# Kernel optimization log

Measured on AMD Instinct MI355X. Metric: run time of the kernel, lower is better.

The kernel has to match this reference:

```python
import jax, jax.numpy as jnp
import numpy as np


def setup_inputs() -> dict:
    key = jax.random.key(0)
    ks = jax.random.split(key, 6)
    B, H, W, C = 4, 56, 56, 256
    NH, K = 8, 7
    return {
        "x": jax.random.normal(ks[0], (B, H, W, C), dtype=jnp.float32),
        "w_qkv": jax.random.normal(ks[1], (C, 3 * C), dtype=jnp.float32) * 0.02,
        "b_qkv": jax.random.normal(ks[2], (3 * C,), dtype=jnp.float32) * 0.02,
        "rpb": jax.random.normal(ks[3], (NH, K * K), dtype=jnp.float32) * 0.02,
        "w_proj": jax.random.normal(ks[4], (C, C), dtype=jnp.float32) * 0.02,
        "b_proj": jax.random.normal(ks[5], (C,), dtype=jnp.float32) * 0.02,
    }


def _window_stack(xp, H, W, ks):
    # xp: (B, H+2p, W+2p, nh, hd) zero-padded map.
    # Returns (B, H, W, nh, ks*ks, hd): each pixel's ks x ks neighborhood,
    # row-major (h offset outer, w offset inner) to match torch unfold order.
    return jnp.stack(
        [xp[:, i:i + H, j:j + W] for i in range(ks) for j in range(ks)],
        axis=-2,
    )


def reference(x, w_qkv, b_qkv, rpb, w_proj, b_proj):
    B, H, W, C = x.shape
    nh, ks2 = rpb.shape
    ks = int(np.sqrt(ks2) + 0.5)  # 7
    hd = C // nh
    scale = hd ** -0.5
    pad = ks // 2  # dilation == 1

    qkv = (x @ w_qkv + b_qkv).reshape(B, H, W, 3, nh, hd)
    q = qkv[..., 0, :, :] * scale        # (B,H,W,nh,hd)
    k = qkv[..., 1, :, :]
    v = qkv[..., 2, :, :]

    pads = ((0, 0), (pad, pad), (pad, pad), (0, 0), (0, 0))
    kw = _window_stack(jnp.pad(k, pads), H, W, ks)  # (B,H,W,nh,ks2,hd)
    vw = _window_stack(jnp.pad(v, pads), H, W, ks)

    # scores over each pixel's ks*ks neighbors (zero-padded borders kept,
    # matching the torch reference), plus relative position bias.
    attn = jnp.einsum("bhwnd,bhwnkd->bhwnk", q, kw) + rpb[None, None, None]
    attn = jax.nn.softmax(attn, axis=-1)
    out = jnp.einsum("bhwnk,bhwnkd->bhwnd", attn, vw).reshape(B, H, W, C)
    return out @ w_proj + b_proj
```

## Files before the change

kernel.cpp:

```cpp
#include <hip/hip_runtime.h>
#include <hip/hip_bf16.h>


using frag_ab = __attribute__((ext_vector_type(8))) short;
using f32x4   = __attribute__((ext_vector_type(4))) float;
using f32x2   = __attribute__((ext_vector_type(2))) float;

typedef const __attribute__((address_space(1))) unsigned int* gas_u32;
typedef __attribute__((address_space(3))) unsigned int*       las_u32;

__device__ __forceinline__ void gl_lds16(const void* g, void* l) {
    __builtin_amdgcn_global_load_lds((gas_u32)g, (las_u32)l, 16, 0, 0);
}

__device__ __forceinline__ float bflo(unsigned int u) { return __uint_as_float(u << 16); }
__device__ __forceinline__ float bfhi(unsigned int u) { return __uint_as_float(u & 0xffff0000u); }

__device__ __forceinline__ f32x2 unpk2(unsigned int u) {
    f32x2 r; r.x = bflo(u); r.y = bfhi(u); return r;
}

#if defined(__has_builtin)
#if __has_builtin(__builtin_amdgcn_fdot2_f32_bf16)
#define HAVE_FDOT2_BF16 1
#endif
#endif

#ifdef HAVE_FDOT2_BF16
typedef __bf16 bf16x2 __attribute__((ext_vector_type(2)));
__device__ __forceinline__ float dot2bf(unsigned int a, unsigned int b, float c) {
    union { unsigned int u; bf16x2 h; } ua, ub;
    ua.u = a; ub.u = b;
    return __builtin_amdgcn_fdot2_f32_bf16(ua.h, ub.h, c, false);
}
#endif

__global__ __launch_bounds__(256) void prep(
    const float* __restrict__ x,      __hip_bfloat16* __restrict__ xb,
    const float* __restrict__ w_qkv,  __hip_bfloat16* __restrict__ wqkvT,
    const float* __restrict__ w_proj, __hip_bfloat16* __restrict__ wprojT,
    __hip_bfloat16* __restrict__ kp,  __hip_bfloat16* __restrict__ vp)
{
    const int bid = blockIdx.x;
    const int tid = threadIdx.x;
    if (bid < 3136) {
        const int i = bid * 256 + tid;
        const float4 v = ((const float4*)x)[i];
        union { ushort4 u; __hip_bfloat16 h[4]; } o;
        o.h[0] = __float2bfloat16(v.x); o.h[1] = __float2bfloat16(v.y);
        o.h[2] = __float2bfloat16(v.z); o.h[3] = __float2bfloat16(v.w);
        ((ushort4*)xb)[i] = o.u;
    } else if (bid < 3904) {
        const int idx = (bid - 3136) * 256 + tid;
        const int k = idx & 255, n = idx >> 8;
        wqkvT[idx] = __float2bfloat16(w_qkv[k * 768 + n]);
    } else if (bid < 4160) {
        const int idx = (bid - 3904) * 256 + tid;
        const int k = idx & 255, n = idx >> 8;
        wprojT[idx] = __float2bfloat16(w_proj[k * 256 + n]);
    } else {
        const int u    = (bid - 4160) * 256 + tid;
        const int ip   = u / 30720;
        const int rem  = u - ip * 30720;
        const int cloc = rem >> 5;
        const int q16  = rem & 31;
        const int img  = ip >> 1;
        __hip_bfloat16* base = (ip & 1) ? vp : kp;
        int prow, pcol;
        if (cloc < 512) {
            const int r8 = cloc >> 6;
            prow = (r8 < 3) ? r8 : r8 + 56;
            pcol = cloc & 63;
        } else {
            const int c2 = cloc - 512;
            prow = 3 + (c2 >> 3);
            const int cc = c2 & 7;
            pcol = (cc < 3) ? cc : cc + 56;
        }
        *(uint4*)(base + (((size_t)(img * 64 + prow)) * 64 + pcol) * 256 + q16 * 8) =
            make_uint4(0u, 0u, 0u, 0u);
    }
}

#define GEMM128_BODY(EPILOGUE)                                                  \
    constexpr int K = 256;                                                      \
    __shared__ frag_ab As[8][64];                                     \
    __shared__ frag_ab Bs[8][64];                                     \
    const int tid  = threadIdx.x;                                               \
    const int lane = tid & 63;                                                  \
    const int w    = tid >> 6;                                                  \
    const int wm   = w >> 1, wn = w & 1;                                        \
    const int m0 = blockIdx.y * 128;                                            \
    const int n0 = blockIdx.x * 128;                                            \
    const int lrow = lane & 15;                                                 \
    const int lk   = (lane >> 4) * 8;                                           \
    const __hip_bfloat16* gA0 = A  + (size_t)(m0 + (2*w+0)*16 + lrow) * K + lk; \
    const __hip_bfloat16* gA1 = A  + (size_t)(m0 + (2*w+1)*16 + lrow) * K + lk; \
    const __hip_bfloat16* gB0 = BT + (size_t)(n0 + (2*w+0)*16 + lrow) * K + lk; \
    const __hip_bfloat16* gB1 = BT + (size_t)(n0 + (2*w+1)*16 + lrow) * K + lk; \
    f32x4 acc[4][4] = {};                                                       \
    for (int k0 = 0; k0 < K; k0 += 32) {                                        \
        gl_lds16(gA0 + k0, &As[2*w+0][0]);                                      \
        gl_lds16(gA1 + k0, &As[2*w+1][0]);                                      \
        gl_lds16(gB0 + k0, &Bs[2*w+0][0]);                                      \
        gl_lds16(gB1 + k0, &Bs[2*w+1][0]);                                      \
        __syncthreads();                                                        \
        frag_ab af[4], bf[4];                                                   \
        _Pragma("unroll")                                                       \
        for (int i = 0; i < 4; ++i) { af[i] = As[wm*4+i][lane]; bf[i] = Bs[wn*4+i][lane]; } \
        _Pragma("unroll")                                                       \
        for (int i = 0; i < 4; ++i)                                             \
            _Pragma("unroll")                                                   \
            for (int j = 0; j < 4; ++j)                                         \
                acc[i][j] = __builtin_amdgcn_mfma_f32_16x16x32_bf16(af[i], bf[j], acc[i][j], 0, 0, 0); \
        __syncthreads();                                                        \
    }                                                                           \
    const int rbase = (lane >> 4) * 4;                                          \
    const int cbase = lane & 15;                                                \
    _Pragma("unroll")                                                           \
    for (int fi = 0; fi < 4; ++fi) {                                            \
        const int rm = m0 + wm * 64 + fi * 16 + rbase;                          \
        _Pragma("unroll")                                                       \
        for (int fj = 0; fj < 4; ++fj) {                                        \
            const int cn = n0 + wn * 64 + fj * 16 + cbase;                      \
            const float bv = bias[cn];                                          \
            _Pragma("unroll")                                                   \
            for (int r = 0; r < 4; ++r) {                                       \
                const int m = rm + r;                                           \
                const float val = acc[fi][fj][r] + bv;                          \
                EPILOGUE                                                        \
            }                                                                   \
        }                                                                       \
    }

__global__ __launch_bounds__(256) void gemm_qkv(
    const __hip_bfloat16* __restrict__ A,
    const __hip_bfloat16* __restrict__ BT,
    const float* __restrict__ bias,
    __hip_bfloat16* __restrict__ qf,
    __hip_bfloat16* __restrict__ kp,
    __hip_bfloat16* __restrict__ vp,
    float qscale)
{
    GEMM128_BODY({
        const int sel = cn >> 8;
        if (sel == 0) {
            qf[(size_t)m * 256 + cn] = __float2bfloat16(val * qscale);
        } else {
            const int c  = cn & 255;
            const int b  = m / 3136;
            const int r2 = m % 3136;
            const int yy = r2 / 56;
            const int xx = r2 % 56;
            __hip_bfloat16* dst = (sel == 1) ? kp : vp;
            dst[(((size_t)(b * 64 + yy + 3)) * 64 + (xx + 3)) * 256 + c] =
                __float2bfloat16(val);
        }
    })
}

__global__ __launch_bounds__(256) void gemm_proj(
    const __hip_bfloat16* __restrict__ A,
    const __hip_bfloat16* __restrict__ BT,
    const float* __restrict__ bias,
    float* __restrict__ C)
{
    constexpr int K = 256;
    __shared__ frag_ab As[4][64];
    __shared__ frag_ab Bs[4][64];

    const int tid  = threadIdx.x;
    const int lane = tid & 63;
    const int w    = tid >> 6;
    const int wm   = w >> 1, wn = w & 1;
    const int m0 = blockIdx.y * 64;
    const int n0 = blockIdx.x * 64;

    const int lrow = lane & 15;
    const int lk   = (lane >> 4) * 8;
    const __hip_bfloat16* gA = A  + (size_t)(m0 + w * 16 + lrow) * K + lk;
    const __hip_bfloat16* gB = BT + (size_t)(n0 + w * 16 + lrow) * K + lk;

    f32x4 acc[2][2] = {};

    for (int k0 = 0; k0 < K; k0 += 32) {
        gl_lds16(gA + k0, &As[w][0]);
        gl_lds16(gB + k0, &Bs[w][0]);
        __syncthreads();
        const frag_ab a0 = As[2 * wm + 0][lane];
        const frag_ab a1 = As[2 * wm + 1][lane];
        const frag_ab b0 = Bs[2 * wn + 0][lane];
        const frag_ab b1 = Bs[2 * wn + 1][lane];
        acc[0][0] = __builtin_amdgcn_mfma_f32_16x16x32_bf16(a0, b0, acc[0][0], 0, 0, 0);
        acc[0][1] = __builtin_amdgcn_mfma_f32_16x16x32_bf16(a0, b1, acc[0][1], 0, 0, 0);
        acc[1][0] = __builtin_amdgcn_mfma_f32_16x16x32_bf16(a1, b0, acc[1][0], 0, 0, 0);
        acc[1][1] = __builtin_amdgcn_mfma_f32_16x16x32_bf16(a1, b1, acc[1][1], 0, 0, 0);
        __syncthreads();
    }

    const int rbase = (lane >> 4) * 4;
    const int cbase = lane & 15;
    #pragma unroll
    for (int fi = 0; fi < 2; ++fi) {
        const int rm = m0 + wm * 32 + fi * 16 + rbase;
        #pragma unroll
        for (int fj = 0; fj < 2; ++fj) {
            const int cn = n0 + wn * 32 + fj * 16 + cbase;
            const float bv = bias[cn];
            #pragma unroll
            for (int r = 0; r < 4; ++r)
                C[(size_t)(rm + r) * 256 + cn] = acc[fi][fj][r] + bv;
        }
    }
}

__global__ __launch_bounds__(64) void na2d_attn11(
    const __hip_bfloat16* __restrict__ qf,
    const __hip_bfloat16* __restrict__ kp,
    const __hip_bfloat16* __restrict__ vp,
    const float* __restrict__ rpb,
    __hip_bfloat16* __restrict__ out)
{
    const int lane = threadIdx.x;
    const int half = lane & 1;
    const int h    = (lane >> 1) & 7;
    const int tl   = (lane >> 4) & 3;

    const int bid = blockIdx.x;
    const int seg = (bid & 7) * 392 + (bid >> 3);
    const int row = seg / 14;
    const int x0  = (seg % 14) * 4;
    const int b   = row / 56;
    const int y   = row % 56;
    const int t   = row * 56 + x0 + tl;
    const int prow0 = b * 64 + y;

    __shared__ __hip_bfloat16 kbuf[10 * 264];
    __shared__ float srpb[8 * 49];

    for (int i = lane; i < 8 * 49; i += 64) srpb[i] = rpb[i];
    __syncthreads();

    unsigned int qpk[8];
    {
        const uint4* qp = (const uint4*)(qf + (size_t)t * 256 + h * 32 + half * 16);
        const uint4 qa = qp[0], qb = qp[1];
        qpk[0] = qa.x; qpk[1] = qa.y; qpk[2] = qa.z; qpk[3] = qa.w;
        qpk[4] = qb.x; qpk[5] = qb.y; qpk[6] = qb.z; qpk[7] = qb.w;
    }
#ifndef HAVE_FDOT2_BF16
    f32x2 q2[8];
    #pragma unroll
    for (int i = 0; i < 8; ++i) q2[i] = unpk2(qpk[i]);
#endif

    const int wroff = (lane >> 5) * 528 + (lane & 31) * 16;
    const int rdoff = tl * 528 + h * 64 + half * 32;

#define GLOAD(plane, ky, d0, d1, d2, d3, d4)                                    \
    do {                                                                        \
        const char* rb_ = (const char*)((plane) +                               \
            ((size_t)(prow0 + (ky)) * 64 + x0) * 256 + lane * 8);               \
        d0 = *(const uint4*)(rb_);                                              \
        d1 = *(const uint4*)(rb_ + 1024);                                       \
        d2 = *(const uint4*)(rb_ + 2048);                                       \
        d3 = *(const uint4*)(rb_ + 3072);                                       \
        d4 = *(const uint4*)(rb_ + 4096);                                       \
    } while (0)

#define LWRITE(buf, s0, s1, s2, s3, s4)                                         \
    do {                                                                        \
        char* wb_ = (char*)(buf) + wroff;                                       \
        *(uint4*)(wb_)        = s0;                                             \
        *(uint4*)(wb_ + 1056) = s1;                                             \
        *(uint4*)(wb_ + 2112) = s2;                                             \
        *(uint4*)(wb_ + 3168) = s3;                                             \
        *(uint4*)(wb_ + 4224) = s4;                                             \
    } while (0)

    const float* rp = &srpb[h * 49];
    float m = -1e30f, l = 0.f;
    f32x2 o2[8] = {};

    uint4 k0, k1, k2, k3, k4;
    GLOAD(kp, 0, k0, k1, k2, k3, k4);

    #pragma unroll 1
    for (int ky = 0; ky < 7; ++ky) {
        LWRITE(kbuf, k0, k1, k2, k3, k4);
        const __hip_bfloat16* vrow = vp +
            ((size_t)(prow0 + ky) * 64 + x0 + tl) * 256 + h * 32 + half * 16;
        uint4 va[7], vb[7];
        #pragma unroll
        for (int kx = 0; kx < 7; ++kx) {
            va[kx] = *(const uint4*)(vrow + kx * 256);
            vb[kx] = *(const uint4*)(vrow + kx * 256 + 8);
        }
        if (ky < 6) GLOAD(kp, ky + 1, k0, k1, k2, k3, k4);
        float lg[7];
        #pragma unroll
        for (int kx = 0; kx < 7; ++kx) {
            const uint4* p = (const uint4*)((const char*)kbuf + rdoff + kx * 528);
            const uint4 w0 = p[0];
            const uint4 w1 = p[1];
#ifdef HAVE_FDOT2_BF16
            float s = 0.f;
            s = dot2bf(qpk[0], w0.x, s);
            s = dot2bf(qpk[1], w0.y, s);
            s = dot2bf(qpk[2], w0.z, s);
            s = dot2bf(qpk[3], w0.w, s);
            s = dot2bf(qpk[4], w1.x, s);
            s = dot2bf(qpk[5], w1.y, s);
            s = dot2bf(qpk[6], w1.z, s);
            s = dot2bf(qpk[7], w1.w, s);
#else
            f32x2 s2 = {0.f, 0.f};
            s2 += q2[0] * unpk2(w0.x);
            s2 += q2[1] * unpk2(w0.y);
            s2 += q2[2] * unpk2(w0.z);
            s2 += q2[3] * unpk2(w0.w);
            s2 += q2[4] * unpk2(w1.x);
            s2 += q2[5] * unpk2(w1.y);
            s2 += q2[6] * unpk2(w1.z);
            s2 += q2[7] * unpk2(w1.w);
            const float s = s2.x + s2.y;
#endif
            lg[kx] = s;
        }
        #pragma unroll
        for (int kx = 0; kx < 7; ++kx) {
            lg[kx] += __shfl_xor(lg[kx], 1, 64);
            lg[kx] += rp[ky * 7 + kx];
        }
        float rmax = lg[0];
        #pragma unroll
        for (int kx = 1; kx < 7; ++kx) rmax = fmaxf(rmax, lg[kx]);
        const float mnew  = fmaxf(m, rmax);
        const float alpha = __expf(m - mnew);
        m = mnew;
        l *= alpha;
        const f32x2 alpha2 = {alpha, alpha};
        #pragma unroll
        for (int i = 0; i < 8; ++i) o2[i] *= alpha2;
        #pragma unroll
        for (int kx = 0; kx < 7; ++kx) {
            const float pr = __expf(lg[kx] - mnew);
            l += pr;
            const f32x2 pr2 = {pr, pr};
            const uint4 w0 = va[kx];
            const uint4 w1 = vb[kx];
            o2[0] += pr2 * unpk2(w0.x);
            o2[1] += pr2 * unpk2(w0.y);
            o2[2] += pr2 * unpk2(w0.z);
            o2[3] += pr2 * unpk2(w0.w);
            o2[4] += pr2 * unpk2(w1.x);
            o2[5] += pr2 * unpk2(w1.y);
            o2[6] += pr2 * unpk2(w1.z);
            o2[7] += pr2 * unpk2(w1.w);
        }
    }
#undef GLOAD
#undef LWRITE

    const float inv = 1.f / l;
    union { uint4 u[2]; __hip_bfloat16 hh[16]; } ob;
    #pragma unroll
    for (int i = 0; i < 8; ++i) {
        ob.hh[2 * i + 0] = __float2bfloat16(o2[i].x * inv);
        ob.hh[2 * i + 1] = __float2bfloat16(o2[i].y * inv);
    }
    uint4* op = (uint4*)(out + (size_t)t * 256 + h * 32 + half * 16);
    op[0] = ob.u[0];
    op[1] = ob.u[1];
}

extern "C" void kernel_launch(void* const* d_in, const int* in_sizes, int n_in,
                              void* d_out, int out_size, void* d_ws, size_t ws_size,
                              hipStream_t stream)
{
    const float* x      = (const float*)d_in[0];
    const float* w_qkv  = (const float*)d_in[1];
    const float* b_qkv  = (const float*)d_in[2];
    const float* rpb    = (const float*)d_in[3];
    const float* w_proj = (const float*)d_in[4];
    const float* b_proj = (const float*)d_in[5];
    float* out = (float*)d_out;

    const int M = 12544;

    char* wsp = (char*)d_ws;
    __hip_bfloat16* qf    = (__hip_bfloat16*)wsp; wsp += (size_t)M * 256 * 2;
    __hip_bfloat16* kp    = (__hip_bfloat16*)wsp; wsp += (size_t)4 * 64 * 64 * 256 * 2;
    __hip_bfloat16* vp    = (__hip_bfloat16*)wsp; wsp += (size_t)4 * 64 * 64 * 256 * 2;
    __hip_bfloat16* xb    = (__hip_bfloat16*)wsp; wsp += (size_t)M * 256 * 2;
    __hip_bfloat16* attnb = (__hip_bfloat16*)wsp; wsp += (size_t)M * 256 * 2;
    __hip_bfloat16* wqkvT = (__hip_bfloat16*)wsp; wsp += (size_t)768 * 256 * 2;
    __hip_bfloat16* wprojT= (__hip_bfloat16*)wsp; wsp += (size_t)256 * 256 * 2;

    const float scale = 0.17677669529663689f;

    prep<<<5120, 256, 0, stream>>>(x, xb, w_qkv, wqkvT, w_proj, wprojT, kp, vp);

    gemm_qkv<<<dim3(6, 98), 256, 0, stream>>>(xb, wqkvT, b_qkv, qf, kp, vp, scale);

    na2d_attn11<<<3136, 64, 0, stream>>>(qf, kp, vp, rpb, attnb);

    gemm_proj<<<dim3(4, 196), 256, 0, stream>>>(attnb, wprojT, b_proj, out);
}
```

Measured before the change: 133.0 us.

## Split head dim across four lanes, two pixels per block in neighborhood attention

Each attention wave now covers 2 pixels instead of 4. Each head's 32-dim slice is split across 4 lanes of 8 elements rather than 2 lanes of 16, and the grid is doubled to 6272 blocks. This halves per-thread registers for V prefetch and accumulators, which may raise occupancy and latency hiding. The cost is an extra cross-lane shuffle per logit and less K-row reuse per block, since each block now loads an 8-pixel row segment to serve 2 outputs instead of 10 for 4.

```diff
diff --git a/kernel.cpp b/kernel.cpp
--- a/kernel.cpp
+++ b/kernel.cpp
@@ -214,7 +214,7 @@
     }
 }
 
-__global__ __launch_bounds__(64) void na2d_attn11(
+__global__ __launch_bounds__(64) void na2d_attn12(
     const __hip_bfloat16* __restrict__ qf,
     const __hip_bfloat16* __restrict__ kp,
     const __hip_bfloat16* __restrict__ vp,
@@ -222,42 +222,40 @@
     __hip_bfloat16* __restrict__ out)
 {
     const int lane = threadIdx.x;
-    const int half = lane & 1;
-    const int h    = (lane >> 1) & 7;
-    const int tl   = (lane >> 4) & 3;
+    const int q8   = lane & 3;
+    const int h    = (lane >> 2) & 7;
+    const int tl   = (lane >> 5) & 1;
 
     const int bid = blockIdx.x;
-    const int seg = (bid & 7) * 392 + (bid >> 3);
-    const int row = seg / 14;
-    const int x0  = (seg % 14) * 4;
+    const int seg = (bid & 7) * 784 + (bid >> 3);
+    const int row = seg / 28;
+    const int x0  = (seg % 28) * 2;
     const int b   = row / 56;
     const int y   = row % 56;
     const int t   = row * 56 + x0 + tl;
     const int prow0 = b * 64 + y;
 
-    __shared__ __hip_bfloat16 kbuf[10 * 264];
+    __shared__ __hip_bfloat16 kbuf[8 * 256];
     __shared__ float srpb[8 * 49];
 
     for (int i = lane; i < 8 * 49; i += 64) srpb[i] = rpb[i];
     __syncthreads();
 
-    unsigned int qpk[8];
+    unsigned int qpk[4];
     {
-        const uint4* qp = (const uint4*)(qf + (size_t)t * 256 + h * 32 + half * 16);
-        const uint4 qa = qp[0], qb = qp[1];
+        const uint4 qa = *(const uint4*)(qf + (size_t)t * 256 + h * 32 + q8 * 8);
         qpk[0] = qa.x; qpk[1] = qa.y; qpk[2] = qa.z; qpk[3] = qa.w;
-        qpk[4] = qb.x; qpk[5] = qb.y; qpk[6] = qb.z; qpk[7] = qb.w;
     }
 #ifndef HAVE_FDOT2_BF16
-    f32x2 q2[8];
+    f32x2 q2[4];
     #pragma unroll
-    for (int i = 0; i < 8; ++i) q2[i] = unpk2(qpk[i]);
-#endif
-
-    const int wroff = (lane >> 5) * 528 + (lane & 31) * 16;
-    const int rdoff = tl * 528 + h * 64 + half * 32;
-
-#define GLOAD(plane, ky, d0, d1, d2, d3, d4)                                    \
+    for (int i = 0; i < 4; ++i) q2[i] = unpk2(qpk[i]);
+#endif
+
+    const int wroff = lane * 16;
+    const int rdoff = tl * 512 + h * 64 + q8 * 16;
+
+#define GLOAD(plane, ky, d0, d1, d2, d3)                                        \
     do {                                                                        \
         const char* rb_ = (const char*)((plane) +                               \
             ((size_t)(prow0 + (ky)) * 64 + x0) * 256 + lane * 8);               \
@@ -265,64 +263,50 @@
         d1 = *(const uint4*)(rb_ + 1024);                                       \
         d2 = *(const uint4*)(rb_ + 2048);                                       \
         d3 = *(const uint4*)(rb_ + 3072);                                       \
-        d4 = *(const uint4*)(rb_ + 4096);                                       \
     } while (0)
 
-#define LWRITE(buf, s0, s1, s2, s3, s4)                                         \
+#define LWRITE(buf, s0, s1, s2, s3)                                             \
     do {                                                                        \
         char* wb_ = (char*)(buf) + wroff;                                       \
         *(uint4*)(wb_)        = s0;                                             \
-        *(uint4*)(wb_ + 1056) = s1;                                             \
-        *(uint4*)(wb_ + 2112) = s2;                                             \
-        *(uint4*)(wb_ + 3168) = s3;                                             \
-        *(uint4*)(wb_ + 4224) = s4;                                             \
+        *(uint4*)(wb_ + 1024) = s1;                                             \
+        *(uint4*)(wb_ + 2048) = s2;                                             \
+        *(uint4*)(wb_ + 3072) = s3;                                             \
     } while (0)
 
     const float* rp = &srpb[h * 49];
     float m = -1e30f, l = 0.f;
-    f32x2 o2[8] = {};
-
-    uint4 k0, k1, k2, k3, k4;
-    GLOAD(kp, 0, k0, k1, k2, k3, k4);
+    f32x2 o2[4] = {};
+
+    uint4 k0, k1, k2, k3;
+    GLOAD(kp, 0, k0, k1, k2, k3);
 
     #pragma unroll 1
     for (int ky = 0; ky < 7; ++ky) {
-        LWRITE(kbuf, k0, k1, k2, k3, k4);
+        LWRITE(kbuf, k0, k1, k2, k3);
         const __hip_bfloat16* vrow = vp +
-            ((size_t)(prow0 + ky) * 64 + x0 + tl) * 256 + h * 32 + half * 16;
-        uint4 va[7], vb[7];
+            ((size_t)(prow0 + ky) * 64 + x0 + tl) * 256 + h * 32 + q8 * 8;
+        uint4 va[7];
+        #pragma unroll
+        for (int kx = 0; kx < 7; ++kx)
+            va[kx] = *(const uint4*)(vrow + kx * 256);
+        if (ky < 6) GLOAD(kp, ky + 1, k0, k1, k2, k3);
+        float lg[7];
         #pragma unroll
         for (int kx = 0; kx < 7; ++kx) {
-            va[kx] = *(const uint4*)(vrow + kx * 256);
-            vb[kx] = *(const uint4*)(vrow + kx * 256 + 8);
-        }
-        if (ky < 6) GLOAD(kp, ky + 1, k0, k1, k2, k3, k4);
-        float lg[7];
-        #pragma unroll
-        for (int kx = 0; kx < 7; ++kx) {
-            const uint4* p = (const uint4*)((const char*)kbuf + rdoff + kx * 528);
-            const uint4 w0 = p[0];
-            const uint4 w1 = p[1];
+            const uint4 w0 = *(const uint4*)((const char*)kbuf + rdoff + kx * 512);
 #ifdef HAVE_FDOT2_BF16
             float s = 0.f;
             s = dot2bf(qpk[0], w0.x, s);
             s = dot2bf(qpk[1], w0.y, s);
             s = dot2bf(qpk[2], w0.z, s);
             s = dot2bf(qpk[3], w0.w, s);
-            s = dot2bf(qpk[4], w1.x, s);
-            s = dot2bf(qpk[5], w1.y, s);
-            s = dot2bf(qpk[6], w1.z, s);
-            s = dot2bf(qpk[7], w1.w, s);
 #else
             f32x2 s2 = {0.f, 0.f};
             s2 += q2[0] * unpk2(w0.x);
             s2 += q2[1] * unpk2(w0.y);
             s2 += q2[2] * unpk2(w0.z);
             s2 += q2[3] * unpk2(w0.w);
-            s2 += q2[4] * unpk2(w1.x);
-            s2 += q2[5] * unpk2(w1.y);
-            s2 += q2[6] * unpk2(w1.z);
-            s2 += q2[7] * unpk2(w1.w);
             const float s = s2.x + s2.y;
 #endif
             lg[kx] = s;
@@ -330,6 +314,7 @@
         #pragma unroll
         for (int kx = 0; kx < 7; ++kx) {
             lg[kx] += __shfl_xor(lg[kx], 1, 64);
+            lg[kx] += __shfl_xor(lg[kx], 2, 64);
             lg[kx] += rp[ky * 7 + kx];
         }
         float rmax = lg[0];
@@ -341,37 +326,30 @@
         l *= alpha;
         const f32x2 alpha2 = {alpha, alpha};
         #pragma unroll
-        for (int i = 0; i < 8; ++i) o2[i] *= alpha2;
+        for (int i = 0; i < 4; ++i) o2[i] *= alpha2;
         #pragma unroll
         for (int kx = 0; kx < 7; ++kx) {
             const float pr = __expf(lg[kx] - mnew);
             l += pr;
             const f32x2 pr2 = {pr, pr};
             const uint4 w0 = va[kx];
-            const uint4 w1 = vb[kx];
             o2[0] += pr2 * unpk2(w0.x);
             o2[1] += pr2 * unpk2(w0.y);
             o2[2] += pr2 * unpk2(w0.z);
             o2[3] += pr2 * unpk2(w0.w);
-            o2[4] += pr2 * unpk2(w1.x);
-            o2[5] += pr2 * unpk2(w1.y);
-            o2[6] += pr2 * unpk2(w1.z);
-            o2[7] += pr2 * unpk2(w1.w);
         }
     }
 #undef GLOAD
 #undef LWRITE
 
     const float inv = 1.f / l;
-    union { uint4 u[2]; __hip_bfloat16 hh[16]; } ob;
+    union { uint4 u; __hip_bfloat16 hh[8]; } ob;
     #pragma unroll
-    for (int i = 0; i < 8; ++i) {
+    for (int i = 0; i < 4; ++i) {
         ob.hh[2 * i + 0] = __float2bfloat16(o2[i].x * inv);
         ob.hh[2 * i + 1] = __float2bfloat16(o2[i].y * inv);
     }
-    uint4* op = (uint4*)(out + (size_t)t * 256 + h * 32 + half * 16);
-    op[0] = ob.u[0];
-    op[1] = ob.u[1];
+    *(uint4*)(out + (size_t)t * 256 + h * 32 + q8 * 8) = ob.u;
 }
 
 extern "C" void kernel_launch(void* const* d_in, const int* in_sizes, int n_in,
@@ -403,7 +381,7 @@
 
     gemm_qkv<<<dim3(6, 98), 256, 0, stream>>>(xb, wqkvT, b_qkv, qf, kp, vp, scale);
 
-    na2d_attn11<<<3136, 64, 0, stream>>>(qf, kp, vp, rpb, attnb);
+    na2d_attn12<<<6272, 64, 0, stream>>>(qf, kp, vp, rpb, attnb);
 
     gemm_proj<<<dim3(4, 196), 256, 0, stream>>>(attnb, wprojT, b_proj, out);
 }
```

New measurement: 133.3 us. No clear change (+0.2%).
